# Kernel optimization log

Measured on AMD Instinct MI355X. Metric: run time of the kernel, lower is better.

Reference implementation:

```python
import jax, jax.numpy as jnp
from jax import lax
import numpy as np

# ---- constants mirroring args ----
T = 8192          # signal length
NUM_CH = 64       # eeg channels
LSTM_SIZE = 256
NUM_CLS = 40
NUM_PROP = 1024   # candidate proposals before NMS
NUM_PROP_AFTER = 256
PROP_LEN = 128    # extracted window length
IOU_THRESH = 0.5


def setup_inputs() -> dict:
    key = jax.random.key(0)
    ks = jax.random.split(key, 12)
    data = jax.random.normal(ks[0], (T, NUM_CH), dtype=jnp.float32)
    # proposals: (start, end, score), 1-D temporal intervals
    starts = jax.random.uniform(ks[1], (NUM_PROP,), minval=0.0, maxval=float(T - PROP_LEN))
    lens = jax.random.uniform(ks[2], (NUM_PROP,), minval=32.0, maxval=float(PROP_LEN))
    scores = jax.random.uniform(ks[3], (NUM_PROP,))
    proposals = jnp.stack([starts, starts + lens, scores], axis=-1).astype(jnp.float32)

    H, C = LSTM_SIZE, NUM_CH
    s_ih = 1.0 / np.sqrt(C)
    s_hh = 1.0 / np.sqrt(H)
    W_ih = jax.random.uniform(ks[4], (4 * H, C), minval=-s_ih, maxval=s_ih)
    W_hh = jax.random.uniform(ks[5], (4 * H, H), minval=-s_hh, maxval=s_hh)
    b_ih = jax.random.uniform(ks[6], (4 * H,), minval=-s_hh, maxval=s_hh)
    b_hh = jax.random.uniform(ks[7], (4 * H,), minval=-s_hh, maxval=s_hh)
    s_h = 1.0 / np.sqrt(H)
    W_cls = jax.random.uniform(ks[8], (NUM_CLS, H), minval=-s_h, maxval=s_h)
    b_cls = jax.random.uniform(ks[9], (NUM_CLS,), minval=-s_h, maxval=s_h)
    W_bbox = jax.random.uniform(ks[10], (2 * NUM_CLS, H), minval=-s_h, maxval=s_h)
    b_bbox = jax.random.uniform(ks[11], (2 * NUM_CLS,), minval=-s_h, maxval=s_h)
    return {"data": data, "proposals": proposals, "W_ih": W_ih, "W_hh": W_hh,
            "b_ih": b_ih, "b_hh": b_hh, "W_cls": W_cls, "b_cls": b_cls,
            "W_bbox": W_bbox, "b_bbox": b_bbox}


def _nms_1d(starts, ends, scores, iou_thresh):
    """Greedy 1-D interval NMS. Returns indices (into original order) of the
    first NUM_PROP_AFTER surviving proposals, in descending-score order."""
    order = jnp.argsort(-scores)
    s, e = starts[order], ends[order]
    n = s.shape[0]
    idx = jnp.arange(n)

    def body(i, sup):
        inter = jnp.maximum(0.0, jnp.minimum(e[i], e) - jnp.maximum(s[i], s))
        union = (e[i] - s[i]) + (e - s) - inter
        iou = inter / jnp.maximum(union, 1e-6)
        new = sup | ((iou > iou_thresh) & (idx > i) & (~sup[i]))
        return new

    suppressed = lax.fori_loop(0, n, body, jnp.zeros(n, dtype=bool))
    keep = ~suppressed
    # stable sort: kept proposals first, preserving score order
    sel = jnp.argsort(jnp.where(keep, 0, 1), stable=True)[:NUM_PROP_AFTER]
    return order[sel]


def _lstm_last(x, W_ih, W_hh, b_ih, b_hh):
    """x: [K, L, C]; returns last hidden state [K, H] (torch gate order ifgo)."""
    K = x.shape[0]
    H = W_hh.shape[1]
    h0 = jnp.zeros((K, H), x.dtype)
    c0 = jnp.zeros((K, H), x.dtype)
    b = b_ih + b_hh

    def step(carry, xt):
        h, c = carry
        gates = xt @ W_ih.T + h @ W_hh.T + b  # [K, 4H]
        i, f, g, o = jnp.split(gates, 4, axis=-1)
        i = jax.nn.sigmoid(i)
        f = jax.nn.sigmoid(f)
        g = jnp.tanh(g)
        o = jax.nn.sigmoid(o)
        c = f * c + i * g
        h = o * jnp.tanh(c)
        return (h, c), None

    (h, _), _ = lax.scan(step, (h0, c0), jnp.swapaxes(x, 0, 1))
    return h


def reference(data, proposals, W_ih, W_hh, b_ih, b_hh, W_cls, b_cls, W_bbox, b_bbox):
    starts, ends, scores = proposals[:, 0], proposals[:, 1], proposals[:, 2]
    # NMS + truncate to num_prop_after (training branch of original)
    kept = _nms_1d(starts, ends, scores, IOU_THRESH)            # [K]
    # extract fixed-length eeg windows at proposal starts (gather)
    t0 = jnp.clip(jnp.round(starts[kept]).astype(jnp.int32), 0, T - PROP_LEN)
    win_idx = t0[:, None] + jnp.arange(PROP_LEN)[None, :]       # [K, L]
    eeg_proposals = data[win_idx]                               # [K, L, C]
    # region LSTM -> last timestep feature
    base_feat = _lstm_last(eeg_proposals, W_ih, W_hh, b_ih, b_hh)  # [K, H]
    cls_feat = base_feat @ W_cls.T + b_cls                      # [K, num_cls]
    bbox_feat = base_feat @ W_bbox.T + b_bbox                   # [K, 2*num_cls]
    return cls_feat, bbox_feat
```

## Files before the change

### kernel.cpp

```cpp
#include <hip/hip_runtime.h>
#include <math.h>

#define T_LEN 8192
#define NUM_CH 64
#define HID 256
#define NUM_CLS 40
#define NUM_PROP 1024
#define NUM_PROP_AFTER 256
#define PROP_LEN 128

#define MS 4
#define NGRP 64
#define NSL 4
#define KH 320
#define KSEGN 4
#define SEGH 80

typedef _Float16 h2_t __attribute__((ext_vector_type(2)));
union U32H2 { unsigned int u; h2_t h; };
union HU16 { _Float16 h; unsigned short u; };

#if defined(__has_builtin)
#if __has_builtin(__builtin_amdgcn_fdot2)
#define HAS_FDOT2 1
#endif
#endif

__device__ __forceinline__ float dot2f(unsigned int wa, unsigned int hb, float acc) {
    U32H2 a, b;
    a.u = wa;
    b.u = hb;
#ifdef HAS_FDOT2
    return __builtin_amdgcn_fdot2(a.h, b.h, acc, false);
#else
    return acc + (float)a.h[0] * (float)b.h[0] + (float)a.h[1] * (float)b.h[1];
#endif
}

__device__ __forceinline__ float dot8f(const uint4& w, const uint4& h, float acc) {
    acc = dot2f(w.x, h.x, acc);
    acc = dot2f(w.y, h.y, acc);
    acc = dot2f(w.z, h.z, acc);
    acc = dot2f(w.w, h.w, acc);
    return acc;
}

__device__ __forceinline__ float fsigmoid(float x) { return 1.0f / (1.0f + __expf(-x)); }
__device__ __forceinline__ float ftanh(float x) {
    float e = __expf(-2.0f * fabsf(x));
    float t = (1.0f - e) / (1.0f + e);
    return copysignf(t, x);
}

__global__ __launch_bounds__(256) void pack_w(const float* __restrict__ W_ih,
                                              const float* __restrict__ W_hh,
                                              unsigned short* __restrict__ WP,
                                              unsigned int* __restrict__ cnt) {
    int e = blockIdx.x * 256 + threadIdx.x;
    int e8 = e & 7;
    int idx = e >> 3;
    int row = idx & 255;
    int t = idx >> 8;
    int j = t % 10;
    int sk = t / 10;
    int kseg = sk & 3;
    int s = sk >> 2;
    int kh = kseg * SEGH + j * 8 + e8;
    int gate = row >> 6, unit = row & 63;
    int grow = gate * 256 + s * 64 + unit;
    float v = (kh < 256) ? W_hh[grow * HID + kh] : W_ih[grow * NUM_CH + (kh - 256)];
    HU16 hv;
    hv.h = (_Float16)v;
    WP[e] = hv.u;
    if (blockIdx.x == 0 && threadIdx.x < NGRP) cnt[threadIdx.x * 16] = 0u;
}

__global__ __launch_bounds__(1024) void nms_kernel(const float* __restrict__ prop,
                                                   int* __restrict__ t0_out) {
    __shared__ float s_sc[NUM_PROP];
    __shared__ float ss[NUM_PROP];
    __shared__ float se[NUM_PROP];
    __shared__ unsigned char sup[NUM_PROP];
    __shared__ unsigned long long cmask[16];

    const int tid = threadIdx.x;
    float ps = prop[tid * 3 + 0];
    float pe = prop[tid * 3 + 1];
    float pc = prop[tid * 3 + 2];
    s_sc[tid] = pc;
    sup[tid] = 0;
    __syncthreads();

    int r = 0;
    for (int j = 0; j < NUM_PROP; ++j) {
        float o = s_sc[j];
        r += (o > pc) || (o == pc && j < tid);
    }
    ss[r] = ps;
    se[r] = pe;
    __syncthreads();

    const float my_s = ss[tid];
    const float my_e = se[tid];
    const float my_len = my_e - my_s;
    bool mysup = false;

    for (int ci = 0; ci < 16; ++ci) {
        if (tid < 64) {
            int i = ci * 64 + tid;
            float is_ = ss[i], ie_ = se[i];
            unsigned long long m = __ballot(sup[i] != 0);
            for (int l = 0; l < 64; ++l) {
                if (!((m >> l) & 1)) {
                    float ls = __shfl(is_, l);
                    float le = __shfl(ie_, l);
                    float inter = fmaxf(fminf(le, ie_) - fmaxf(ls, is_), 0.0f);
                    float uni = (le - ls) + (ie_ - is_) - inter;
                    float iou = inter / fmaxf(uni, 1e-6f);
                    unsigned long long nb = __ballot((tid > l) && (iou > 0.5f));
                    m |= nb;
                }
            }
            sup[i] = (unsigned char)((m >> tid) & 1);
            if (tid == 0) cmask[ci] = ~m;
        }
        __syncthreads();
        unsigned long long am = cmask[ci];
        for (int l = 0; l < 64; ++l) {
            if ((am >> l) & 1) {
                int i = ci * 64 + l;
                if (tid > i && !mysup) {
                    float ls = ss[i], le = se[i];
                    float inter = fmaxf(fminf(le, my_e) - fmaxf(ls, my_s), 0.0f);
                    float uni = (le - ls) + my_len - inter;
                    if (inter / fmaxf(uni, 1e-6f) > 0.5f) mysup = true;
                }
            }
        }
        sup[tid] = mysup ? 1 : 0;
        __syncthreads();
    }

    int myc = tid >> 6;
    unsigned long long mybit = 1ull << (tid & 63);
    int kb = 0, kt = 0;
    for (int c2 = 0; c2 < 16; ++c2) {
        int p = __popcll(cmask[c2]);
        kt += p;
        if (c2 < myc) kb += p;
    }
    kb += __popcll(cmask[myc] & (mybit - 1));
    int slot = (cmask[myc] & mybit) ? kb : (kt + (tid - kb));
    if (slot < NUM_PROP_AFTER) {
        int t0 = (int)rintf(my_s);
        t0 = max(0, min(t0, T_LEN - PROP_LEN));
        t0_out[slot] = t0;
    }
}

__global__ __launch_bounds__(1024, 4) void lstm_kernel(
    const float* __restrict__ data, const int* __restrict__ t0s,
    const unsigned short* __restrict__ WP,
    const float* __restrict__ b_ih, const float* __restrict__ b_hh,
    const float* __restrict__ W_cls, const float* __restrict__ b_cls,
    const float* __restrict__ W_bbox, const float* __restrict__ b_bbox,
    float* __restrict__ out, unsigned int* __restrict__ Hx,
    unsigned int* __restrict__ cnt) {
    __shared__ __align__(16) _Float16 hx[MS][KH];
    __shared__ float pp[MS][KSEGN][256];

    const int tid = threadIdx.x;
    const int g = blockIdx.x & (NGRP - 1);
    const int s = blockIdx.x >> 6;
    const int kseg = tid >> 8;
    const int rl = tid & 255;

    uint4 Wr[10];
    {
        const uint4* wp4 = (const uint4*)WP;
        int base = ((s * 4 + kseg) * 10) * 256 + rl;
#pragma unroll
        for (int j = 0; j < 10; ++j) Wr[j] = wp4[base + j * 256];
    }

    const int aq = tid >> 6;
    const int au = tid & 63;
    float bi = 0.f, bf = 0.f, bg = 0.f, bo = 0.f, c_st = 0.f;
    if (tid < 256) {
        int u = s * 64 + au;
        bi = b_ih[u] + b_hh[u];
        bf = b_ih[256 + u] + b_hh[256 + u];
        bg = b_ih[512 + u] + b_hh[512 + u];
        bo = b_ih[768 + u] + b_hh[768 + u];
    }

    const int xs = (tid >> 6) & 3;
    const int xch = tid & 63;
    const bool xrole = (tid >= 512 && tid < 768);
    int xt0 = 0;
    if (xrole) {
        xt0 = t0s[g * MS + xs];
        hx[xs][256 + xch] = (_Float16)data[xt0 * NUM_CH + xch];
    }
    hx[tid >> 8][tid & 255] = (_Float16)0.0f;

    unsigned short* HxH = (unsigned short*)Hx;
    unsigned int* cg = &cnt[g * 16];
    __syncthreads();

    for (int t = 0; t < PROP_LEN; ++t) {
        float a0 = 0.f, a1 = 0.f, a2 = 0.f, a3 = 0.f;
#pragma unroll
        for (int j = 0; j < 10; ++j) {
            const int hb = kseg * SEGH + j * 8;
            uint4 h0 = *(const uint4*)&hx[0][hb];
            uint4 h1 = *(const uint4*)&hx[1][hb];
            uint4 h2 = *(const uint4*)&hx[2][hb];
            uint4 h3 = *(const uint4*)&hx[3][hb];
            uint4 w = Wr[j];
            a0 = dot8f(w, h0, a0);
            a1 = dot8f(w, h1, a1);
            a2 = dot8f(w, h2, a2);
            a3 = dot8f(w, h3, a3);
        }
        pp[0][kseg][rl] = a0;
        pp[1][kseg][rl] = a1;
        pp[2][kseg][rl] = a2;
        pp[3][kseg][rl] = a3;
        __syncthreads();

        if (tid < 256) {
            float si = pp[aq][0][au] + pp[aq][1][au] + pp[aq][2][au] +
                       pp[aq][3][au] + bi;
            float sf = pp[aq][0][64 + au] + pp[aq][1][64 + au] +
                       pp[aq][2][64 + au] + pp[aq][3][64 + au] + bf;
            float sg = pp[aq][0][128 + au] + pp[aq][1][128 + au] +
                       pp[aq][2][128 + au] + pp[aq][3][128 + au] + bg;
            float so = pp[aq][0][192 + au] + pp[aq][1][192 + au] +
                       pp[aq][2][192 + au] + pp[aq][3][192 + au] + bo;
            float gi = fsigmoid(si), gf = fsigmoid(sf);
            float gg = ftanh(sg), go = fsigmoid(so);
            c_st = gf * c_st + gi * gg;
            float h = go * ftanh(c_st);
            HU16 hu;
            hu.h = (_Float16)h;
            __hip_atomic_store(
                &HxH[((((t + 1) & 1) * NGRP + g) * MS + aq) * 256 + s * 64 + au],
                hu.u, __ATOMIC_RELAXED, __HIP_MEMORY_SCOPE_AGENT);
            asm volatile("s_waitcnt vmcnt(0)" ::: "memory");
            if (au == 0)
                __hip_atomic_fetch_add(cg, 1u, __ATOMIC_RELAXED,
                                       __HIP_MEMORY_SCOPE_AGENT);
        } else if (xrole && t + 1 < PROP_LEN) {
            hx[xs][256 + xch] = (_Float16)data[(xt0 + t + 1) * NUM_CH + xch];
        }

        const unsigned int tgt = 16u * (unsigned int)(t + 1);
        if (tid == 0) {
            while (__hip_atomic_load(cg, __ATOMIC_RELAXED,
                                     __HIP_MEMORY_SCOPE_AGENT) < tgt) {
                __builtin_amdgcn_s_sleep(1);
            }
        }
        __syncthreads();
        if (tid < 512) {
            int sq = tid >> 7, w = tid & 127;
            unsigned int v = __hip_atomic_load(
                &Hx[((((t + 1) & 1) * NGRP + g) * MS + sq) * 128 + w],
                __ATOMIC_RELAXED, __HIP_MEMORY_SCOPE_AGENT);
            ((unsigned int*)hx)[sq * 160 + w] = v;
        }
        __syncthreads();
    }

    if (tid < MS * 30) {
        int sq = tid / 30;
        int ml = tid % 30;
        int m = s * 30 + ml;
        const float* Wrow;
        float acc;
        int oidx;
        if (m < NUM_CLS) {
            Wrow = W_cls + m * HID;
            acc = b_cls[m];
            oidx = (g * MS + sq) * NUM_CLS + m;
        } else {
            int mb = m - NUM_CLS;
            Wrow = W_bbox + mb * HID;
            acc = b_bbox[mb];
            oidx = NUM_PROP_AFTER * NUM_CLS + (g * MS + sq) * 2 * NUM_CLS + mb;
        }
        const float4* w4 = (const float4*)Wrow;
        const _Float16* hp = &hx[sq][0];
        for (int c = 0; c < 32; ++c) {
            float4 wa = w4[c * 2 + 0];
            float4 wb = w4[c * 2 + 1];
            acc += (float)hp[c * 8 + 0] * wa.x + (float)hp[c * 8 + 1] * wa.y +
                   (float)hp[c * 8 + 2] * wa.z + (float)hp[c * 8 + 3] * wa.w +
                   (float)hp[c * 8 + 4] * wb.x + (float)hp[c * 8 + 5] * wb.y +
                   (float)hp[c * 8 + 6] * wb.z + (float)hp[c * 8 + 7] * wb.w;
        }
        out[oidx] = acc;
    }
}

extern "C" void kernel_launch(void* const* d_in, const int* in_sizes, int n_in,
                              void* d_out, int out_size, void* d_ws,
                              size_t ws_size, hipStream_t stream) {
    const float* data = (const float*)d_in[0];
    const float* prop = (const float*)d_in[1];
    const float* W_ih = (const float*)d_in[2];
    const float* W_hh = (const float*)d_in[3];
    const float* b_ih = (const float*)d_in[4];
    const float* b_hh = (const float*)d_in[5];
    const float* W_cls = (const float*)d_in[6];
    const float* b_cls = (const float*)d_in[7];
    const float* W_bbox = (const float*)d_in[8];
    const float* b_bbox = (const float*)d_in[9];
    float* out = (float*)d_out;

    int* t0s = (int*)d_ws;
    unsigned short* WP = (unsigned short*)((char*)d_ws + 1024);
    unsigned int* Hx = (unsigned int*)((char*)d_ws + 656384);
    unsigned int* cnt = (unsigned int*)((char*)d_ws + 918528);

    pack_w<<<1280, 256, 0, stream>>>(W_ih, W_hh, WP, cnt);
    nms_kernel<<<1, 1024, 0, stream>>>(prop, t0s);

    void* kargs[] = {(void*)&data, (void*)&t0s,    (void*)&WP,    (void*)&b_ih,
                     (void*)&b_hh, (void*)&W_cls,  (void*)&b_cls, (void*)&W_bbox,
                     (void*)&b_bbox, (void*)&out,  (void*)&Hx,    (void*)&cnt};
    hipLaunchCooperativeKernel((void*)lstm_kernel, dim3(NSL * NGRP), dim3(1024),
                               kargs, 0, stream);
}
```

Before: 740.1 us.

## Fuse NMS and weight packing into cooperative LSTM kernel with per-slice flags

Removes the separate pack_w and nms_kernel launches. Block 0 now runs NMS inside the cooperative LSTM kernel and publishes the t0 values through a global flag, and each block converts its fp32 weights to fp16 registers directly from W_hh/W_ih. The per-step group barrier changes from one atomic counter polled by a single thread to per-slice counters polled by a waiting wavefront, and h is copied back with 64-bit loads. The cost is that every block waits on block 0's serial NMS, and a memset is added to clear the counters.

Result: slower. 762.6 us (+3.0%).

```diff
diff --git a/kernel.cpp b/kernel.cpp
--- a/kernel.cpp
+++ b/kernel.cpp
@@ -52,122 +52,24 @@
     return copysignf(t, x);
 }
 
-__global__ __launch_bounds__(256) void pack_w(const float* __restrict__ W_ih,
-                                              const float* __restrict__ W_hh,
-                                              unsigned short* __restrict__ WP,
-                                              unsigned int* __restrict__ cnt) {
-    int e = blockIdx.x * 256 + threadIdx.x;
-    int e8 = e & 7;
-    int idx = e >> 3;
-    int row = idx & 255;
-    int t = idx >> 8;
-    int j = t % 10;
-    int sk = t / 10;
-    int kseg = sk & 3;
-    int s = sk >> 2;
-    int kh = kseg * SEGH + j * 8 + e8;
-    int gate = row >> 6, unit = row & 63;
-    int grow = gate * 256 + s * 64 + unit;
-    float v = (kh < 256) ? W_hh[grow * HID + kh] : W_ih[grow * NUM_CH + (kh - 256)];
-    HU16 hv;
-    hv.h = (_Float16)v;
-    WP[e] = hv.u;
-    if (blockIdx.x == 0 && threadIdx.x < NGRP) cnt[threadIdx.x * 16] = 0u;
-}
-
-__global__ __launch_bounds__(1024) void nms_kernel(const float* __restrict__ prop,
-                                                   int* __restrict__ t0_out) {
-    __shared__ float s_sc[NUM_PROP];
-    __shared__ float ss[NUM_PROP];
-    __shared__ float se[NUM_PROP];
-    __shared__ unsigned char sup[NUM_PROP];
-    __shared__ unsigned long long cmask[16];
-
-    const int tid = threadIdx.x;
-    float ps = prop[tid * 3 + 0];
-    float pe = prop[tid * 3 + 1];
-    float pc = prop[tid * 3 + 2];
-    s_sc[tid] = pc;
-    sup[tid] = 0;
-    __syncthreads();
-
-    int r = 0;
-    for (int j = 0; j < NUM_PROP; ++j) {
-        float o = s_sc[j];
-        r += (o > pc) || (o == pc && j < tid);
-    }
-    ss[r] = ps;
-    se[r] = pe;
-    __syncthreads();
-
-    const float my_s = ss[tid];
-    const float my_e = se[tid];
-    const float my_len = my_e - my_s;
-    bool mysup = false;
-
-    for (int ci = 0; ci < 16; ++ci) {
-        if (tid < 64) {
-            int i = ci * 64 + tid;
-            float is_ = ss[i], ie_ = se[i];
-            unsigned long long m = __ballot(sup[i] != 0);
-            for (int l = 0; l < 64; ++l) {
-                if (!((m >> l) & 1)) {
-                    float ls = __shfl(is_, l);
-                    float le = __shfl(ie_, l);
-                    float inter = fmaxf(fminf(le, ie_) - fmaxf(ls, is_), 0.0f);
-                    float uni = (le - ls) + (ie_ - is_) - inter;
-                    float iou = inter / fmaxf(uni, 1e-6f);
-                    unsigned long long nb = __ballot((tid > l) && (iou > 0.5f));
-                    m |= nb;
-                }
-            }
-            sup[i] = (unsigned char)((m >> tid) & 1);
-            if (tid == 0) cmask[ci] = ~m;
-        }
-        __syncthreads();
-        unsigned long long am = cmask[ci];
-        for (int l = 0; l < 64; ++l) {
-            if ((am >> l) & 1) {
-                int i = ci * 64 + l;
-                if (tid > i && !mysup) {
-                    float ls = ss[i], le = se[i];
-                    float inter = fmaxf(fminf(le, my_e) - fmaxf(ls, my_s), 0.0f);
-                    float uni = (le - ls) + my_len - inter;
-                    if (inter / fmaxf(uni, 1e-6f) > 0.5f) mysup = true;
-                }
-            }
-        }
-        sup[tid] = mysup ? 1 : 0;
-        __syncthreads();
-    }
-
-    int myc = tid >> 6;
-    unsigned long long mybit = 1ull << (tid & 63);
-    int kb = 0, kt = 0;
-    for (int c2 = 0; c2 < 16; ++c2) {
-        int p = __popcll(cmask[c2]);
-        kt += p;
-        if (c2 < myc) kb += p;
-    }
-    kb += __popcll(cmask[myc] & (mybit - 1));
-    int slot = (cmask[myc] & mybit) ? kb : (kt + (tid - kb));
-    if (slot < NUM_PROP_AFTER) {
-        int t0 = (int)rintf(my_s);
-        t0 = max(0, min(t0, T_LEN - PROP_LEN));
-        t0_out[slot] = t0;
-    }
-}
-
-__global__ __launch_bounds__(1024, 4) void lstm_kernel(
-    const float* __restrict__ data, const int* __restrict__ t0s,
-    const unsigned short* __restrict__ WP,
+__device__ __forceinline__ unsigned int pack2(float a, float b) {
+    HU16 ha, hb;
+    ha.h = (_Float16)a;
+    hb.h = (_Float16)b;
+    return (unsigned int)ha.u | ((unsigned int)hb.u << 16);
+}
+
+__global__ __launch_bounds__(1024, 4) void fused_kernel(
+    const float* __restrict__ data, const float* __restrict__ prop,
+    const float* __restrict__ W_ih, const float* __restrict__ W_hh,
     const float* __restrict__ b_ih, const float* __restrict__ b_hh,
     const float* __restrict__ W_cls, const float* __restrict__ b_cls,
     const float* __restrict__ W_bbox, const float* __restrict__ b_bbox,
-    float* __restrict__ out, unsigned int* __restrict__ Hx,
-    unsigned int* __restrict__ cnt) {
+    float* __restrict__ out, int* __restrict__ t0s,
+    unsigned int* __restrict__ Hx, unsigned int* __restrict__ cnt,
+    unsigned int* __restrict__ flag) {
     __shared__ __align__(16) _Float16 hx[MS][KH];
-    __shared__ float pp[MS][KSEGN][256];
+    __shared__ __align__(16) float pp[MS][KSEGN][256];
 
     const int tid = threadIdx.x;
     const int g = blockIdx.x & (NGRP - 1);
@@ -175,12 +77,110 @@
     const int kseg = tid >> 8;
     const int rl = tid & 255;
 
+    if (blockIdx.x == 0) {
+        float* sc_p = &pp[0][0][0];
+        float* ss = &pp[1][0][0];
+        float* se = &pp[2][0][0];
+        unsigned char* sup = (unsigned char*)&pp[3][0][0];
+        unsigned long long* cmask =
+            (unsigned long long*)((char*)&pp[3][0][0] + 1024);
+
+        float ps = prop[tid * 3 + 0];
+        float pe = prop[tid * 3 + 1];
+        float pc = prop[tid * 3 + 2];
+        sc_p[tid] = pc;
+        sup[tid] = 0;
+        __syncthreads();
+
+        int r = 0;
+        for (int j = 0; j < NUM_PROP; ++j) {
+            float o = sc_p[j];
+            r += (o > pc) || (o == pc && j < tid);
+        }
+        ss[r] = ps;
+        se[r] = pe;
+        __syncthreads();
+
+        const float my_s = ss[tid];
+        const float my_e = se[tid];
+        const float my_len = my_e - my_s;
+        bool mysup = false;
+
+        for (int ci = 0; ci < 16; ++ci) {
+            if (tid < 64) {
+                int i = ci * 64 + tid;
+                float is_ = ss[i], ie_ = se[i];
+                unsigned long long m = __ballot(sup[i] != 0);
+                for (int l = 0; l < 64; ++l) {
+                    if (!((m >> l) & 1)) {
+                        float ls = __shfl(is_, l);
+                        float le = __shfl(ie_, l);
+                        float inter = fmaxf(fminf(le, ie_) - fmaxf(ls, is_), 0.0f);
+                        float uni = (le - ls) + (ie_ - is_) - inter;
+                        float iou = inter / fmaxf(uni, 1e-6f);
+                        unsigned long long nb = __ballot((tid > l) && (iou > 0.5f));
+                        m |= nb;
+                    }
+                }
+                sup[i] = (unsigned char)((m >> tid) & 1);
+                if (tid == 0) cmask[ci] = ~m;
+            }
+            __syncthreads();
+            unsigned long long am = cmask[ci];
+            for (int l = 0; l < 64; ++l) {
+                if ((am >> l) & 1) {
+                    int i = ci * 64 + l;
+                    if (tid > i && !mysup) {
+                        float ls = ss[i], le = se[i];
+                        float inter = fmaxf(fminf(le, my_e) - fmaxf(ls, my_s), 0.0f);
+                        float uni = (le - ls) + my_len - inter;
+                        if (inter / fmaxf(uni, 1e-6f) > 0.5f) mysup = true;
+                    }
+                }
+            }
+            sup[tid] = mysup ? 1 : 0;
+            __syncthreads();
+        }
+
+        int myc = tid >> 6;
+        unsigned long long mybit = 1ull << (tid & 63);
+        int kb = 0, kt = 0;
+        for (int c2 = 0; c2 < 16; ++c2) {
+            int p = __popcll(cmask[c2]);
+            kt += p;
+            if (c2 < myc) kb += p;
+        }
+        kb += __popcll(cmask[myc] & (mybit - 1));
+        int slot = (cmask[myc] & mybit) ? kb : (kt + (tid - kb));
+        if (slot < NUM_PROP_AFTER) {
+            int t0v = (int)rintf(my_s);
+            t0v = max(0, min(t0v, T_LEN - PROP_LEN));
+            __hip_atomic_store(&t0s[slot], t0v, __ATOMIC_RELAXED,
+                               __HIP_MEMORY_SCOPE_AGENT);
+        }
+        asm volatile("s_waitcnt vmcnt(0)" ::: "memory");
+        __syncthreads();
+        if (tid == 0)
+            __hip_atomic_store(flag, 1u, __ATOMIC_RELAXED,
+                               __HIP_MEMORY_SCOPE_AGENT);
+        __syncthreads();
+    }
+
     uint4 Wr[10];
     {
-        const uint4* wp4 = (const uint4*)WP;
-        int base = ((s * 4 + kseg) * 10) * 256 + rl;
+        const int gate = rl >> 6, unit = rl & 63;
+        const int grow = gate * 256 + s * 64 + unit;
+        const float* __restrict__ baseh = W_hh + grow * HID;
+        const float* __restrict__ basex = W_ih + grow * NUM_CH;
 #pragma unroll
-        for (int j = 0; j < 10; ++j) Wr[j] = wp4[base + j * 256];
+        for (int j = 0; j < 10; ++j) {
+            const int kh = kseg * SEGH + j * 8;
+            const float* src = (kh < 256) ? (baseh + kh) : (basex + (kh - 256));
+            float4 f0 = *(const float4*)(src);
+            float4 f1 = *(const float4*)(src + 4);
+            Wr[j] = make_uint4(pack2(f0.x, f0.y), pack2(f0.z, f0.w),
+                               pack2(f1.x, f1.y), pack2(f1.z, f1.w));
+        }
     }
 
     const int aq = tid >> 6;
@@ -194,18 +194,29 @@
         bo = b_ih[768 + u] + b_hh[768 + u];
     }
 
+    hx[tid >> 8][tid & 255] = (_Float16)0.0f;
+
+    if (tid == 0) {
+        while (__hip_atomic_load(flag, __ATOMIC_RELAXED,
+                                 __HIP_MEMORY_SCOPE_AGENT) == 0u) {
+            __builtin_amdgcn_s_sleep(4);
+        }
+    }
+    __syncthreads();
+
     const int xs = (tid >> 6) & 3;
     const int xch = tid & 63;
-    const bool xrole = (tid >= 512 && tid < 768);
     int xt0 = 0;
-    if (xrole) {
-        xt0 = t0s[g * MS + xs];
+    if (tid >= 768) {
+        xt0 = __hip_atomic_load(&t0s[g * MS + xs], __ATOMIC_RELAXED,
+                                __HIP_MEMORY_SCOPE_AGENT);
         hx[xs][256 + xch] = (_Float16)data[xt0 * NUM_CH + xch];
     }
-    hx[tid >> 8][tid & 255] = (_Float16)0.0f;
 
     unsigned short* HxH = (unsigned short*)Hx;
+    unsigned long long* Hx64 = (unsigned long long*)Hx;
     unsigned int* cg = &cnt[g * 16];
+    const int pi = tid & 15;
     __syncthreads();
 
     for (int t = 0; t < PROP_LEN; ++t) {
@@ -229,6 +240,7 @@
         pp[3][kseg][rl] = a3;
         __syncthreads();
 
+        const unsigned int tgt = (unsigned int)(t + 1);
         if (tid < 256) {
             float si = pp[aq][0][au] + pp[aq][1][au] + pp[aq][2][au] +
                        pp[aq][3][au] + bi;
@@ -249,26 +261,23 @@
                 hu.u, __ATOMIC_RELAXED, __HIP_MEMORY_SCOPE_AGENT);
             asm volatile("s_waitcnt vmcnt(0)" ::: "memory");
             if (au == 0)
-                __hip_atomic_fetch_add(cg, 1u, __ATOMIC_RELAXED,
-                                       __HIP_MEMORY_SCOPE_AGENT);
-        } else if (xrole && t + 1 < PROP_LEN) {
-            hx[xs][256 + xch] = (_Float16)data[(xt0 + t + 1) * NUM_CH + xch];
-        }
-
-        const unsigned int tgt = 16u * (unsigned int)(t + 1);
-        if (tid == 0) {
-            while (__hip_atomic_load(cg, __ATOMIC_RELAXED,
-                                     __HIP_MEMORY_SCOPE_AGENT) < tgt) {
-                __builtin_amdgcn_s_sleep(1);
-            }
-        }
-        __syncthreads();
-        if (tid < 512) {
-            int sq = tid >> 7, w = tid & 127;
-            unsigned int v = __hip_atomic_load(
-                &Hx[((((t + 1) & 1) * NGRP + g) * MS + sq) * 128 + w],
+                __hip_atomic_store(&cg[s * 4 + aq], tgt, __ATOMIC_RELAXED,
+                                   __HIP_MEMORY_SCOPE_AGENT);
+        } else if (tid < 512) {
+            unsigned int v;
+            do {
+                v = __hip_atomic_load(&cg[pi], __ATOMIC_RELAXED,
+                                      __HIP_MEMORY_SCOPE_AGENT);
+            } while (__any(v < tgt));
+            int gi2 = tid - 256;
+            int sq = gi2 >> 6, w2 = gi2 & 63;
+            unsigned long long hv = __hip_atomic_load(
+                &Hx64[((((t + 1) & 1) * NGRP + g) * MS + sq) * 64 + w2],
                 __ATOMIC_RELAXED, __HIP_MEMORY_SCOPE_AGENT);
-            ((unsigned int*)hx)[sq * 160 + w] = v;
+            ((unsigned long long*)&hx[sq][0])[w2] = hv;
+        } else if (tid >= 768) {
+            if (t + 1 < PROP_LEN)
+                hx[xs][256 + xch] = (_Float16)data[(xt0 + t + 1) * NUM_CH + xch];
         }
         __syncthreads();
     }
@@ -320,16 +329,16 @@
     float* out = (float*)d_out;
 
     int* t0s = (int*)d_ws;
-    unsigned short* WP = (unsigned short*)((char*)d_ws + 1024);
-    unsigned int* Hx = (unsigned int*)((char*)d_ws + 656384);
-    unsigned int* cnt = (unsigned int*)((char*)d_ws + 918528);
-
-    pack_w<<<1280, 256, 0, stream>>>(W_ih, W_hh, WP, cnt);
-    nms_kernel<<<1, 1024, 0, stream>>>(prop, t0s);
-
-    void* kargs[] = {(void*)&data, (void*)&t0s,    (void*)&WP,    (void*)&b_ih,
-                     (void*)&b_hh, (void*)&W_cls,  (void*)&b_cls, (void*)&W_bbox,
-                     (void*)&b_bbox, (void*)&out,  (void*)&Hx,    (void*)&cnt};
-    hipLaunchCooperativeKernel((void*)lstm_kernel, dim3(NSL * NGRP), dim3(1024),
+    unsigned int* Hx = (unsigned int*)((char*)d_ws + 1024);
+    unsigned int* cnt = (unsigned int*)((char*)d_ws + 263168);
+    unsigned int* flag = (unsigned int*)((char*)d_ws + 267264);
+
+    hipMemsetAsync((char*)d_ws + 263168, 0, 4096 + 64, stream);
+
+    void* kargs[] = {(void*)&data,  (void*)&prop,   (void*)&W_ih,  (void*)&W_hh,
+                     (void*)&b_ih,  (void*)&b_hh,   (void*)&W_cls, (void*)&b_cls,
+                     (void*)&W_bbox, (void*)&b_bbox, (void*)&out,  (void*)&t0s,
+                     (void*)&Hx,    (void*)&cnt,    (void*)&flag};
+    hipLaunchCooperativeKernel((void*)fused_kernel, dim3(NSL * NGRP), dim3(1024),
                                kargs, 0, stream);
 }
```
